# Performance work log

Measured on AMD Instinct MI355X. Metric: run time of the kernel, lower is better.

Reference implementation:

```python
import jax, jax.numpy as jnp
import numpy as np

V, B, C, NS, H, W = 3, 2, 64, 32, 128, 128


def setup_inputs() -> dict:
    key = jax.random.key(0)
    k1, k2 = jax.random.split(key, 2)
    features = jax.random.normal(k1, (V, B, C, H, W), dtype=jnp.float32)
    f = 1.1 * W
    K = np.array([[f, 0.0, (W - 1) / 2.0],
                  [0.0, f, (H - 1) / 2.0],
                  [0.0, 0.0, 1.0]], dtype=np.float32)
    intrinsics = jnp.asarray(np.broadcast_to(K, (V, B, 3, 3)).copy())
    c2w = np.tile(np.eye(4, dtype=np.float32), (V, B, 1, 1))
    rng = np.random.default_rng(0)
    for v in range(1, V):
        for b in range(B):
            th = rng.uniform(-0.03, 0.03)
            Ry = np.array([[np.cos(th), 0.0, np.sin(th)],
                           [0.0, 1.0, 0.0],
                           [-np.sin(th), 0.0, np.cos(th)]], dtype=np.float32)
            c2w[v, b, :3, :3] = Ry
            c2w[v, b, :3, 3] = rng.uniform(-0.1, 0.1, size=3).astype(np.float32)
    cam_to_world = jnp.asarray(c2w)
    scale_hypo = jnp.broadcast_to(jnp.linspace(0.5, 1.5, NS, dtype=jnp.float32), (B, NS)) + jnp.zeros((B, NS), jnp.float32)
    depth_init = 2.0 + 4.0 * jax.random.uniform(k2, (B, H, W), dtype=jnp.float32)
    return {"features": features, "intrinsics": intrinsics, "cam_to_world": cam_to_world,
            "scale_hypo": scale_hypo, "depth_init": depth_init}


def _grid_sample_zeros(feat, grid):
    """torch F.grid_sample(mode='bilinear', padding_mode='zeros', align_corners=False)."""
    Bn, Cn, Hn, Wn = feat.shape
    ix = ((grid[..., 0] + 1.0) * Wn - 1.0) * 0.5
    iy = ((grid[..., 1] + 1.0) * Hn - 1.0) * 0.5
    x0 = jnp.floor(ix); y0 = jnp.floor(iy)
    x1 = x0 + 1.0; y1 = y0 + 1.0
    wx1 = ix - x0; wx0 = 1.0 - wx1
    wy1 = iy - y0; wy0 = 1.0 - wy1
    featf = feat.reshape(Bn, Cn, Hn * Wn)

    def corner(xc, yc, w):
        valid = (xc >= 0) & (xc <= Wn - 1) & (yc >= 0) & (yc <= Hn - 1)
        xi = jnp.clip(xc, 0, Wn - 1).astype(jnp.int32)
        yi = jnp.clip(yc, 0, Hn - 1).astype(jnp.int32)
        idx = (yi * Wn + xi).reshape(Bn, 1, -1)
        v = jnp.take_along_axis(featf, idx, axis=2)  # (B,C,Npts)
        return v * (w * valid).reshape(Bn, 1, -1)

    out = (corner(x0, y0, wx0 * wy0) + corner(x1, y0, wx1 * wy0)
           + corner(x0, y1, wx0 * wy1) + corner(x1, y1, wx1 * wy1))
    return out.reshape(Bn, Cn, grid.shape[1], grid.shape[2])


def _homo_warp(src_feat, scale_hypo, depth_init, src_K, src_c2w, ref_K, ref_c2w):
    # src_feat (B,C,H,W); depth_init (B,1,H,W); returns (B,C,Ns,H,W)
    Bn, Cn, Hn, Wn = src_feat.shape
    Ns = scale_hypo.shape[1]

    def build_grid():
        src_w2c = jnp.linalg.inv(src_c2w)
        ref_w2c = jnp.linalg.inv(ref_c2w)
        # original clones world_to_cam and only replaces the top-left 3x3 with K,
        # so the w2c translation column is kept inside the 'intrinsics' matrix
        src_P = src_w2c.at[:, :3, :3].set(src_K)
        ref_P = ref_w2c.at[:, :3, :3].set(ref_K)
        proj = (src_P @ src_w2c) @ jnp.linalg.inv(ref_P @ ref_w2c)
        rot = proj[:, :3, :3]
        trans = proj[:, :3, 3]
        depth = depth_init.reshape(Bn, 1, 1, Hn * Wn) * scale_hypo[:, None, :, None]  # (B,1,Ns,HW)
        # NOTE: original builds both grid axes from arange(height); valid since H==W
        y, x = jnp.meshgrid(jnp.arange(Hn, dtype=jnp.float32),
                            jnp.arange(Wn, dtype=jnp.float32), indexing='ij')
        xyz = jnp.stack([x.ravel(), y.ravel(), jnp.ones(Hn * Wn, dtype=jnp.float32)])  # (3,HW)
        rot_xyz = jnp.einsum('bij,jn->bin', rot, xyz)                         # (B,3,HW)
        proj_xyz = rot_xyz[:, :, None, :] * depth + trans[:, :, None, None]   # (B,3,Ns,HW)
        proj_xy = proj_xyz[:, :2] / proj_xyz[:, 2:3]
        gx = proj_xy[:, 0] / ((Wn - 1) / 2.0) - 1.0
        gy = proj_xy[:, 1] / ((Hn - 1) / 2.0) - 1.0
        return jnp.stack([gx, gy], axis=-1).reshape(Bn, Ns * Hn, Wn, 2)

    grid = jax.lax.stop_gradient(build_grid())  # torch computes the grid under no_grad
    warped = _grid_sample_zeros(src_feat, grid)
    return warped.reshape(Bn, Cn, Ns, Hn, Wn)


def reference(features, intrinsics, cam_to_world, scale_hypo, depth_init):
    num_views = features.shape[0]
    Bn, Cn, Hn, Wn = features.shape[1:]
    Ns = scale_hypo.shape[1]
    ref_K, ref_c2w = intrinsics[0], cam_to_world[0]
    # faithfully replicate torch's in-place ref_volume.sub_() bug:
    # ref accumulates the subtraction of every previously-warped volume
    ref_running = jnp.broadcast_to(features[0][:, :, None], (Bn, Cn, Ns, Hn, Wn))
    cost = jnp.zeros((Bn, Ns, Hn, Wn), dtype=features.dtype)
    for v in range(1, num_views):
        warped = _homo_warp(features[v], scale_hypo, depth_init[:, None],
                            intrinsics[v], cam_to_world[v], ref_K, ref_c2w)
        ref_running = ref_running - warped
        cost = cost + jnp.sqrt(jnp.sum(ref_running * ref_running, axis=1))  # L2 over C
    cost = cost / (num_views - 1)
    cost = jnp.mean(cost, axis=(2, 3))          # (B, Nscale)
    prob = jax.nn.softmax(cost, axis=1)
    return jnp.sum(prob * scale_hypo, axis=1)   # (B,)
```

## Files before the change

### kernel.cpp

```cpp
#include <hip/hip_runtime.h>
#include <math.h>

constexpr int NV = 3;
constexpr int NB = 2;
constexpr int NC = 64;
constexpr int NSC = 32;
constexpr int NH = 128;
constexpr int NW = 128;
constexpr int NSB = 4;

template <int CTRL>
__device__ __forceinline__ float dpp_add(float x) {
    int s = __builtin_amdgcn_update_dpp(0, __float_as_int(x), CTRL, 0xf, 0xf, true);
    return x + __int_as_float(s);
}

__device__ __forceinline__ void conv8(const uint4& q, float* o) {
    o[0] = __uint_as_float(q.x << 16);
    o[1] = __uint_as_float(q.x & 0xFFFF0000u);
    o[2] = __uint_as_float(q.y << 16);
    o[3] = __uint_as_float(q.y & 0xFFFF0000u);
    o[4] = __uint_as_float(q.z << 16);
    o[5] = __uint_as_float(q.z & 0xFFFF0000u);
    o[6] = __uint_as_float(q.w << 16);
    o[7] = __uint_as_float(q.w & 0xFFFF0000u);
}

__device__ __forceinline__ unsigned int f32_to_bf16_rne(float f) {
    unsigned int u = __float_as_uint(f);
    u += 0x7fffu + ((u >> 16) & 1u);
    return u >> 16;
}

__device__ void inv4x4(const double* m, double* out) {
    double inv[16];
    inv[0]  =  m[5]*m[10]*m[15] - m[5]*m[11]*m[14] - m[9]*m[6]*m[15] + m[9]*m[7]*m[14] + m[13]*m[6]*m[11] - m[13]*m[7]*m[10];
    inv[4]  = -m[4]*m[10]*m[15] + m[4]*m[11]*m[14] + m[8]*m[6]*m[15] - m[8]*m[7]*m[14] - m[12]*m[6]*m[11] + m[12]*m[7]*m[10];
    inv[8]  =  m[4]*m[9]*m[15]  - m[4]*m[11]*m[13] - m[8]*m[5]*m[15] + m[8]*m[7]*m[13] + m[12]*m[5]*m[11] - m[12]*m[7]*m[9];
    inv[12] = -m[4]*m[9]*m[14]  + m[4]*m[10]*m[13] + m[8]*m[5]*m[14] - m[8]*m[6]*m[13] - m[12]*m[5]*m[10] + m[12]*m[6]*m[9];
    inv[1]  = -m[1]*m[10]*m[15] + m[1]*m[11]*m[14] + m[9]*m[2]*m[15] - m[9]*m[3]*m[14] - m[13]*m[2]*m[11] + m[13]*m[3]*m[10];
    inv[5]  =  m[0]*m[10]*m[15] - m[0]*m[11]*m[14] - m[8]*m[2]*m[15] + m[8]*m[3]*m[14] + m[12]*m[2]*m[11] - m[12]*m[3]*m[10];
    inv[9]  = -m[0]*m[9]*m[15]  + m[0]*m[11]*m[13] + m[8]*m[1]*m[15] - m[8]*m[3]*m[13] - m[12]*m[1]*m[11] + m[12]*m[3]*m[9];
    inv[13] =  m[0]*m[9]*m[14]  - m[0]*m[10]*m[13] - m[8]*m[1]*m[14] + m[8]*m[2]*m[13] + m[12]*m[1]*m[10] - m[12]*m[2]*m[9];
    inv[2]  =  m[1]*m[6]*m[15]  - m[1]*m[7]*m[14]  - m[5]*m[2]*m[15] + m[5]*m[3]*m[14] + m[13]*m[2]*m[7]  - m[13]*m[3]*m[6];
    inv[6]  = -m[0]*m[6]*m[15]  + m[0]*m[7]*m[14]  + m[4]*m[2]*m[15] - m[4]*m[3]*m[14] - m[12]*m[2]*m[7]  + m[12]*m[3]*m[6];
    inv[10] =  m[0]*m[5]*m[15]  - m[0]*m[7]*m[13]  - m[4]*m[1]*m[15] + m[4]*m[3]*m[13] + m[12]*m[1]*m[7]  - m[12]*m[3]*m[5];
    inv[14] = -m[0]*m[5]*m[14]  + m[0]*m[6]*m[13]  + m[4]*m[1]*m[14] - m[4]*m[2]*m[13] - m[12]*m[1]*m[6]  + m[12]*m[2]*m[5];
    inv[3]  = -m[1]*m[6]*m[11]  + m[1]*m[7]*m[10]  + m[5]*m[2]*m[11] - m[5]*m[3]*m[10] - m[9]*m[2]*m[7]   + m[9]*m[3]*m[6];
    inv[7]  =  m[0]*m[6]*m[11]  - m[0]*m[7]*m[10]  - m[4]*m[2]*m[11] + m[4]*m[3]*m[10] + m[8]*m[2]*m[7]   - m[8]*m[3]*m[6];
    inv[11] = -m[0]*m[5]*m[11]  + m[0]*m[7]*m[9]   + m[4]*m[1]*m[11] - m[4]*m[3]*m[9]  - m[8]*m[1]*m[7]   + m[8]*m[3]*m[5];
    inv[15] =  m[0]*m[5]*m[10]  - m[0]*m[6]*m[9]   - m[4]*m[1]*m[10] + m[4]*m[2]*m[9]  + m[8]*m[1]*m[6]   - m[8]*m[2]*m[5];
    double det = m[0]*inv[0] + m[1]*inv[4] + m[2]*inv[8] + m[3]*inv[12];
    det = 1.0 / det;
    for (int i = 0; i < 16; ++i) out[i] = inv[i] * det;
}

__device__ void mat4mul(const double* a, const double* b, double* o) {
    for (int i = 0; i < 4; ++i)
        for (int j = 0; j < 4; ++j) {
            double s = 0.0;
            for (int k = 0; k < 4; ++k) s += a[i*4+k] * b[k*4+j];
            o[i*4+j] = s;
        }
}

__global__ void setup_kernel(const float* __restrict__ intr,
                             const float* __restrict__ c2w,
                             float* __restrict__ rt,
                             float* __restrict__ cost) {
    int t = threadIdx.x;
    if (t >= 4 && t < 4 + NB * NSC) cost[t - 4] = 0.f;
    if (t >= 2 * NB) return;
    int vi = t >> 1;
    int b  = t & 1;
    int v  = vi + 1;

    double src_c2w[16], ref_c2w[16];
    for (int i = 0; i < 16; ++i) {
        src_c2w[i] = (double)c2w[(v * NB + b) * 16 + i];
        ref_c2w[i] = (double)c2w[(0 * NB + b) * 16 + i];
    }
    double src_w2c[16], ref_w2c[16];
    inv4x4(src_c2w, src_w2c);
    inv4x4(ref_c2w, ref_w2c);

    double srcP[16], refP[16];
    for (int i = 0; i < 16; ++i) { srcP[i] = src_w2c[i]; refP[i] = ref_w2c[i]; }
    for (int r = 0; r < 3; ++r)
        for (int c = 0; c < 3; ++c) {
            srcP[r*4+c] = (double)intr[(v * NB + b) * 9 + r*3 + c];
            refP[r*4+c] = (double)intr[(0 * NB + b) * 9 + r*3 + c];
        }

    double M1[16], M2[16], M2inv[16];
    mat4mul(srcP, src_w2c, M1);
    mat4mul(refP, ref_w2c, M2);
    inv4x4(M2, M2inv);
    double proj[16];
    mat4mul(M1, M2inv, proj);

    float* o = rt + (vi * NB + b) * 12;
    o[0] = (float)proj[0];  o[1] = (float)proj[1];  o[2]  = (float)proj[2];
    o[3] = (float)proj[4];  o[4] = (float)proj[5];  o[5]  = (float)proj[6];
    o[6] = (float)proj[8];  o[7] = (float)proj[9];  o[8]  = (float)proj[10];
    o[9] = (float)proj[3];  o[10] = (float)proj[7]; o[11] = (float)proj[11];
}

__global__ __launch_bounds__(256) void transpose_kernel(const float* __restrict__ in,
                                                        unsigned int* __restrict__ out) {
    __shared__ float tile[NC][NW + 1];
    const int y  = blockIdx.x;
    const int vb = blockIdx.y;

    for (int i = threadIdx.x; i < NC * NW; i += 256) {
        int c = i >> 7;
        int x = i & (NW - 1);
        tile[c][x] = in[((size_t)(vb * NC + c) * NH + y) * NW + x];
    }
    __syncthreads();
    unsigned int* dst = out + ((size_t)vb * NH + y) * NW * (NC / 2);
    for (int i = threadIdx.x; i < NW * (NC / 2); i += 256) {
        int x  = i >> 5;
        int cp = i & 31;
        unsigned int lo = f32_to_bf16_rne(tile[2 * cp][x]);
        unsigned int hi = f32_to_bf16_rne(tile[2 * cp + 1][x]);
        dst[x * (NC / 2) + cp] = lo | (hi << 16);
    }
}

__global__ __launch_bounds__(256) void cost_kernel(
    const unsigned int* __restrict__ ftb,
    const float* __restrict__ depth,
    const float* __restrict__ scale,
    const float* __restrict__ rt,
    float* __restrict__ cost)
{
    const int tid  = threadIdx.x;
    const int lane = tid & 63;
    const int wv   = tid >> 6;
    const int grp  = lane >> 3;
    const int gl   = lane & 7;
    const int nsg  = blockIdx.y;
    const int b    = blockIdx.z;

    const int p = blockIdx.x * 32 + wv * 8 + grp;
    const int x = p & (NW - 1);
    const int y = p >> 7;
    const float fx = (float)x;
    const float fy = (float)y;

    const float d0 = depth[(b * NH + y) * NW + x];

    const uint4* f0q = (const uint4*)(ftb) + ((size_t)(0 * NB + b) * NH * NW + p) * 8 + gl;
    const uint4* v1q = (const uint4*)(ftb) + ((size_t)(1 * NB + b) * NH * NW) * 8 + gl;
    const uint4* v2q = (const uint4*)(ftb) + ((size_t)(2 * NB + b) * NH * NW) * 8 + gl;

    float f0c[8];
    conv8(*f0q, f0c);

    float R0[12], R1[12];
#pragma unroll
    for (int k = 0; k < 12; ++k) {
        R0[k] = rt[(0 * NB + b) * 12 + k];
        R1[k] = rt[(1 * NB + b) * 12 + k];
    }
    const float ax0 = R0[0] * fx + R0[1] * fy + R0[2];
    const float ay0 = R0[3] * fx + R0[4] * fy + R0[5];
    const float az0 = R0[6] * fx + R0[7] * fy + R0[8];
    const float ax1 = R1[0] * fx + R1[1] * fy + R1[2];
    const float ay1 = R1[3] * fx + R1[4] * fy + R1[5];
    const float az1 = R1[6] * fx + R1[7] * fy + R1[8];

    const float CXY = 64.0f / 63.5f;

    __shared__ float red[4][NSB];
    float outv[NSB];

#pragma unroll
    for (int nsub = 0; nsub < NSB; ++nsub) {
        const float s = scale[b * NSC + nsg * NSB + nsub];
        const float d = d0 * s;

        int   ti[2][4];
        float tw[2][4];
#pragma unroll
        for (int vi = 0; vi < 2; ++vi) {
            float px = (vi ? ax1 : ax0) * d + (vi ? R1[9]  : R0[9]);
            float py = (vi ? ay1 : ay0) * d + (vi ? R1[10] : R0[10]);
            float pz = (vi ? az1 : az0) * d + (vi ? R1[11] : R0[11]);
            float invz = __builtin_amdgcn_rcpf(pz);
            float ix = (px * invz) * CXY - 0.5f;
            float iy = (py * invz) * CXY - 0.5f;

            float x0f = floorf(ix), y0f = floorf(iy);
            float wx1 = ix - x0f, wx0 = 1.f - wx1;
            float wy1 = iy - y0f, wy0 = 1.f - wy1;

            float mx0 = (x0f >= 0.f  && x0f <= 127.f) ? wx0 : 0.f;
            float mx1 = (x0f >= -1.f && x0f <= 126.f) ? wx1 : 0.f;
            float my0 = (y0f >= 0.f  && y0f <= 127.f) ? wy0 : 0.f;
            float my1 = (y0f >= -1.f && y0f <= 126.f) ? wy1 : 0.f;

            int xi0 = (int)fminf(fmaxf(x0f, 0.f), 127.f);
            int yi0 = (int)fminf(fmaxf(y0f, 0.f), 127.f);
            int xo = (x0f >= 0.f && x0f <= 126.f) ? 8 : 0;
            int yo = (y0f >= 0.f && y0f <= 126.f) ? NW * 8 : 0;

            int base = (yi0 * NW + xi0) * 8;
            ti[vi][0] = base;
            ti[vi][1] = base + xo;
            ti[vi][2] = base + yo;
            ti[vi][3] = base + yo + xo;
            tw[vi][0] = mx0 * my0;
            tw[vi][1] = mx1 * my0;
            tw[vi][2] = mx0 * my1;
            tw[vi][3] = mx1 * my1;
        }

        uint4 t0 = v1q[ti[0][0]];
        uint4 t1 = v1q[ti[0][1]];
        uint4 t2 = v1q[ti[0][2]];
        uint4 t3 = v1q[ti[0][3]];
        uint4 u0 = v2q[ti[1][0]];
        uint4 u1 = v2q[ti[1][1]];
        uint4 u2 = v2q[ti[1][2]];
        uint4 u3 = v2q[ti[1][3]];

        float c8[8], acc[8], r[8];

        conv8(t0, acc);
#pragma unroll
        for (int k = 0; k < 8; ++k) acc[k] *= tw[0][0];
        conv8(t1, c8);
#pragma unroll
        for (int k = 0; k < 8; ++k) acc[k] += c8[k] * tw[0][1];
        conv8(t2, c8);
#pragma unroll
        for (int k = 0; k < 8; ++k) acc[k] += c8[k] * tw[0][2];
        conv8(t3, c8);
#pragma unroll
        for (int k = 0; k < 8; ++k) acc[k] += c8[k] * tw[0][3];

        float sq1 = 0.f;
#pragma unroll
        for (int k = 0; k < 8; ++k) {
            r[k] = f0c[k] - acc[k];
            sq1 += r[k] * r[k];
        }

        conv8(u0, acc);
#pragma unroll
        for (int k = 0; k < 8; ++k) acc[k] *= tw[1][0];
        conv8(u1, c8);
#pragma unroll
        for (int k = 0; k < 8; ++k) acc[k] += c8[k] * tw[1][1];
        conv8(u2, c8);
#pragma unroll
        for (int k = 0; k < 8; ++k) acc[k] += c8[k] * tw[1][2];
        conv8(u3, c8);
#pragma unroll
        for (int k = 0; k < 8; ++k) acc[k] += c8[k] * tw[1][3];

        float sq2 = 0.f;
#pragma unroll
        for (int k = 0; k < 8; ++k) {
            r[k] -= acc[k];
            sq2 += r[k] * r[k];
        }

        sq1 = dpp_add<0x111>(sq1);
        sq1 = dpp_add<0x112>(sq1);
        sq1 = dpp_add<0x114>(sq1);
        sq2 = dpp_add<0x111>(sq2);
        sq2 = dpp_add<0x112>(sq2);
        sq2 = dpp_add<0x114>(sq2);
        float sv = sqrtf(sq1) + sqrtf(sq2);
        sv = dpp_add<0x118>(sv);
        sv = dpp_add<0x142>(sv);
        sv = dpp_add<0x143>(sv);
        outv[nsub] = sv;
    }

    if (lane == 63) {
#pragma unroll
        for (int nsub = 0; nsub < NSB; ++nsub) red[wv][nsub] = outv[nsub];
    }
    __syncthreads();
    if (tid < NSB) {
        float t = red[0][tid] + red[1][tid] + red[2][tid] + red[3][tid];
        atomicAdd(&cost[b * NSC + nsg * NSB + tid], t * (0.5f / (float)(NH * NW)));
    }
}

__global__ void finalize_kernel(const float* __restrict__ cost,
                                const float* __restrict__ scale,
                                float* __restrict__ out) {
    int tid = threadIdx.x;
    if (tid >= NB * NSC) return;
    int b = tid >> 5;
    int ns = tid & 31;
    float c = cost[b * NSC + ns];
    float sv = scale[b * NSC + ns];

    float m = c;
#pragma unroll
    for (int mk = 1; mk < 32; mk <<= 1) m = fmaxf(m, __shfl_xor(m, mk, 64));
    float e = __expf(c - m);
    float sum = e;
#pragma unroll
    for (int mk = 1; mk < 32; mk <<= 1) sum += __shfl_xor(sum, mk, 64);
    float val = (e / sum) * sv;
#pragma unroll
    for (int mk = 1; mk < 32; mk <<= 1) val += __shfl_xor(val, mk, 64);
    if (ns == 0) out[b] = val;
}

extern "C" void kernel_launch(void* const* d_in, const int* in_sizes, int n_in,
                              void* d_out, int out_size, void* d_ws, size_t ws_size,
                              hipStream_t stream) {
    const float* features   = (const float*)d_in[0];
    const float* intrinsics = (const float*)d_in[1];
    const float* cam2world  = (const float*)d_in[2];
    const float* scale_hypo = (const float*)d_in[3];
    const float* depth_init = (const float*)d_in[4];
    float* out = (float*)d_out;

    unsigned int* ftb = (unsigned int*)d_ws;
    float* rt   = (float*)(ftb + (size_t)NV * NB * NH * NW * (NC / 2));
    float* cost = rt + 2 * NB * 12;

    setup_kernel<<<1, 128, 0, stream>>>(intrinsics, cam2world, rt, cost);

    dim3 tgrid(NH, NV * NB);
    transpose_kernel<<<tgrid, 256, 0, stream>>>(features, ftb);

    dim3 cgrid(NH * NW / 32, NSC / NSB, NB);
    cost_kernel<<<cgrid, 256, 0, stream>>>(ftb, depth_init, scale_hypo, rt, cost);

    finalize_kernel<<<1, 64, 0, stream>>>(cost, scale_hypo, out);
}
```

Measured before the change: 187.8 us.

## Switch feature staging to fp16 with packed math and fold setup into transpose

Features are now stored as packed fp16 instead of bf16, and the bilinear interpolation and residual run in packed half2 arithmetic. Squared norms use the fdot2 instruction, which removes the per-element unpack to fp32. The separate setup kernel that computes the projection matrices and zeroes the cost buffer is merged into one block of the transpose kernel, saving a launch. The cost is lower precision: interpolation now accumulates in fp16 and the weights are rounded to fp16.

Result: faster. 166.0 us (-11.6%).

```diff
diff --git a/kernel.cpp b/kernel.cpp
--- a/kernel.cpp
+++ b/kernel.cpp
@@ -9,27 +9,21 @@
 constexpr int NW = 128;
 constexpr int NSB = 4;
 
+typedef _Float16 h2_t __attribute__((ext_vector_type(2)));
+
 template <int CTRL>
 __device__ __forceinline__ float dpp_add(float x) {
     int s = __builtin_amdgcn_update_dpp(0, __float_as_int(x), CTRL, 0xf, 0xf, true);
     return x + __int_as_float(s);
 }
 
-__device__ __forceinline__ void conv8(const uint4& q, float* o) {
-    o[0] = __uint_as_float(q.x << 16);
-    o[1] = __uint_as_float(q.x & 0xFFFF0000u);
-    o[2] = __uint_as_float(q.y << 16);
-    o[3] = __uint_as_float(q.y & 0xFFFF0000u);
-    o[4] = __uint_as_float(q.z << 16);
-    o[5] = __uint_as_float(q.z & 0xFFFF0000u);
-    o[6] = __uint_as_float(q.w << 16);
-    o[7] = __uint_as_float(q.w & 0xFFFF0000u);
-}
-
-__device__ __forceinline__ unsigned int f32_to_bf16_rne(float f) {
-    unsigned int u = __float_as_uint(f);
-    u += 0x7fffu + ((u >> 16) & 1u);
-    return u >> 16;
+__device__ __forceinline__ float dot2acc(h2_t a, float acc) {
+#if __has_builtin(__builtin_amdgcn_fdot2)
+    return __builtin_amdgcn_fdot2(a, a, acc, false);
+#else
+    float x = (float)a.x, y = (float)a.y;
+    return acc + x * x + y * y;
+#endif
 }
 
 __device__ void inv4x4(const double* m, double* out) {
@@ -64,50 +58,12 @@
         }
 }
 
-__global__ void setup_kernel(const float* __restrict__ intr,
-                             const float* __restrict__ c2w,
-                             float* __restrict__ rt,
-                             float* __restrict__ cost) {
-    int t = threadIdx.x;
-    if (t >= 4 && t < 4 + NB * NSC) cost[t - 4] = 0.f;
-    if (t >= 2 * NB) return;
-    int vi = t >> 1;
-    int b  = t & 1;
-    int v  = vi + 1;
-
-    double src_c2w[16], ref_c2w[16];
-    for (int i = 0; i < 16; ++i) {
-        src_c2w[i] = (double)c2w[(v * NB + b) * 16 + i];
-        ref_c2w[i] = (double)c2w[(0 * NB + b) * 16 + i];
-    }
-    double src_w2c[16], ref_w2c[16];
-    inv4x4(src_c2w, src_w2c);
-    inv4x4(ref_c2w, ref_w2c);
-
-    double srcP[16], refP[16];
-    for (int i = 0; i < 16; ++i) { srcP[i] = src_w2c[i]; refP[i] = ref_w2c[i]; }
-    for (int r = 0; r < 3; ++r)
-        for (int c = 0; c < 3; ++c) {
-            srcP[r*4+c] = (double)intr[(v * NB + b) * 9 + r*3 + c];
-            refP[r*4+c] = (double)intr[(0 * NB + b) * 9 + r*3 + c];
-        }
-
-    double M1[16], M2[16], M2inv[16];
-    mat4mul(srcP, src_w2c, M1);
-    mat4mul(refP, ref_w2c, M2);
-    inv4x4(M2, M2inv);
-    double proj[16];
-    mat4mul(M1, M2inv, proj);
-
-    float* o = rt + (vi * NB + b) * 12;
-    o[0] = (float)proj[0];  o[1] = (float)proj[1];  o[2]  = (float)proj[2];
-    o[3] = (float)proj[4];  o[4] = (float)proj[5];  o[5]  = (float)proj[6];
-    o[6] = (float)proj[8];  o[7] = (float)proj[9];  o[8]  = (float)proj[10];
-    o[9] = (float)proj[3];  o[10] = (float)proj[7]; o[11] = (float)proj[11];
-}
-
 __global__ __launch_bounds__(256) void transpose_kernel(const float* __restrict__ in,
-                                                        unsigned int* __restrict__ out) {
+                                                        unsigned int* __restrict__ out,
+                                                        const float* __restrict__ intr,
+                                                        const float* __restrict__ c2w,
+                                                        float* __restrict__ rt,
+                                                        float* __restrict__ cost) {
     __shared__ float tile[NC][NW + 1];
     const int y  = blockIdx.x;
     const int vb = blockIdx.y;
@@ -122,9 +78,48 @@
     for (int i = threadIdx.x; i < NW * (NC / 2); i += 256) {
         int x  = i >> 5;
         int cp = i & 31;
-        unsigned int lo = f32_to_bf16_rne(tile[2 * cp][x]);
-        unsigned int hi = f32_to_bf16_rne(tile[2 * cp + 1][x]);
-        dst[x * (NC / 2) + cp] = lo | (hi << 16);
+        h2_t h = { (_Float16)tile[2 * cp][x], (_Float16)tile[2 * cp + 1][x] };
+        dst[x * (NC / 2) + cp] = __builtin_bit_cast(unsigned int, h);
+    }
+
+    if (blockIdx.x == 0 && blockIdx.y == 0) {
+        int t = threadIdx.x;
+        if (t >= 4 && t < 4 + NB * NSC) cost[t - 4] = 0.f;
+        if (t < 2 * NB) {
+            int vi = t >> 1;
+            int b  = t & 1;
+            int v  = vi + 1;
+
+            double src_c2w[16], ref_c2w[16];
+            for (int i = 0; i < 16; ++i) {
+                src_c2w[i] = (double)c2w[(v * NB + b) * 16 + i];
+                ref_c2w[i] = (double)c2w[(0 * NB + b) * 16 + i];
+            }
+            double src_w2c[16], ref_w2c[16];
+            inv4x4(src_c2w, src_w2c);
+            inv4x4(ref_c2w, ref_w2c);
+
+            double srcP[16], refP[16];
+            for (int i = 0; i < 16; ++i) { srcP[i] = src_w2c[i]; refP[i] = ref_w2c[i]; }
+            for (int r = 0; r < 3; ++r)
+                for (int c = 0; c < 3; ++c) {
+                    srcP[r*4+c] = (double)intr[(v * NB + b) * 9 + r*3 + c];
+                    refP[r*4+c] = (double)intr[(0 * NB + b) * 9 + r*3 + c];
+                }
+
+            double M1[16], M2[16], M2inv[16];
+            mat4mul(srcP, src_w2c, M1);
+            mat4mul(refP, ref_w2c, M2);
+            inv4x4(M2, M2inv);
+            double proj[16];
+            mat4mul(M1, M2inv, proj);
+
+            float* o = rt + (vi * NB + b) * 12;
+            o[0] = (float)proj[0];  o[1] = (float)proj[1];  o[2]  = (float)proj[2];
+            o[3] = (float)proj[4];  o[4] = (float)proj[5];  o[5]  = (float)proj[6];
+            o[6] = (float)proj[8];  o[7] = (float)proj[9];  o[8]  = (float)proj[10];
+            o[9] = (float)proj[3];  o[10] = (float)proj[7]; o[11] = (float)proj[11];
+        }
     }
 }
 
@@ -155,8 +150,8 @@
     const uint4* v1q = (const uint4*)(ftb) + ((size_t)(1 * NB + b) * NH * NW) * 8 + gl;
     const uint4* v2q = (const uint4*)(ftb) + ((size_t)(2 * NB + b) * NH * NW) * 8 + gl;
 
-    float f0c[8];
-    conv8(*f0q, f0c);
+    const uint4 f0u = *f0q;
+    const h2_t* f0h = (const h2_t*)&f0u;
 
     float R0[12], R1[12];
 #pragma unroll
@@ -226,46 +221,42 @@
         uint4 u2 = v2q[ti[1][2]];
         uint4 u3 = v2q[ti[1][3]];
 
-        float c8[8], acc[8], r[8];
-
-        conv8(t0, acc);
-#pragma unroll
-        for (int k = 0; k < 8; ++k) acc[k] *= tw[0][0];
-        conv8(t1, c8);
-#pragma unroll
-        for (int k = 0; k < 8; ++k) acc[k] += c8[k] * tw[0][1];
-        conv8(t2, c8);
-#pragma unroll
-        for (int k = 0; k < 8; ++k) acc[k] += c8[k] * tw[0][2];
-        conv8(t3, c8);
-#pragma unroll
-        for (int k = 0; k < 8; ++k) acc[k] += c8[k] * tw[0][3];
-
-        float sq1 = 0.f;
-#pragma unroll
-        for (int k = 0; k < 8; ++k) {
-            r[k] = f0c[k] - acc[k];
-            sq1 += r[k] * r[k];
-        }
-
-        conv8(u0, acc);
-#pragma unroll
-        for (int k = 0; k < 8; ++k) acc[k] *= tw[1][0];
-        conv8(u1, c8);
-#pragma unroll
-        for (int k = 0; k < 8; ++k) acc[k] += c8[k] * tw[1][1];
-        conv8(u2, c8);
-#pragma unroll
-        for (int k = 0; k < 8; ++k) acc[k] += c8[k] * tw[1][2];
-        conv8(u3, c8);
-#pragma unroll
-        for (int k = 0; k < 8; ++k) acc[k] += c8[k] * tw[1][3];
-
-        float sq2 = 0.f;
-#pragma unroll
-        for (int k = 0; k < 8; ++k) {
-            r[k] -= acc[k];
-            sq2 += r[k] * r[k];
+        _Float16 w00 = (_Float16)(-tw[0][0]), w01 = (_Float16)(-tw[0][1]);
+        _Float16 w02 = (_Float16)(-tw[0][2]), w03 = (_Float16)(-tw[0][3]);
+        _Float16 w10 = (_Float16)(-tw[1][0]), w11 = (_Float16)(-tw[1][1]);
+        _Float16 w12 = (_Float16)(-tw[1][2]), w13 = (_Float16)(-tw[1][3]);
+        h2_t h00 = {w00, w00}, h01 = {w01, w01}, h02 = {w02, w02}, h03 = {w03, w03};
+        h2_t h10 = {w10, w10}, h11 = {w11, w11}, h12 = {w12, w12}, h13 = {w13, w13};
+
+        const h2_t* p0 = (const h2_t*)&t0;
+        const h2_t* p1 = (const h2_t*)&t1;
+        const h2_t* p2 = (const h2_t*)&t2;
+        const h2_t* p3 = (const h2_t*)&t3;
+        const h2_t* q0 = (const h2_t*)&u0;
+        const h2_t* q1 = (const h2_t*)&u1;
+        const h2_t* q2 = (const h2_t*)&u2;
+        const h2_t* q3 = (const h2_t*)&u3;
+
+        h2_t r[4];
+        float sq1 = 0.f, sq2 = 0.f;
+#pragma unroll
+        for (int j = 0; j < 4; ++j) {
+            h2_t rr = f0h[j];
+            rr += p0[j] * h00;
+            rr += p1[j] * h01;
+            rr += p2[j] * h02;
+            rr += p3[j] * h03;
+            r[j] = rr;
+            sq1 = dot2acc(rr, sq1);
+        }
+#pragma unroll
+        for (int j = 0; j < 4; ++j) {
+            h2_t rr = r[j];
+            rr += q0[j] * h10;
+            rr += q1[j] * h11;
+            rr += q2[j] * h12;
+            rr += q3[j] * h13;
+            sq2 = dot2acc(rr, sq2);
         }
 
         sq1 = dpp_add<0x111>(sq1);
@@ -329,10 +320,8 @@
     float* rt   = (float*)(ftb + (size_t)NV * NB * NH * NW * (NC / 2));
     float* cost = rt + 2 * NB * 12;
 
-    setup_kernel<<<1, 128, 0, stream>>>(intrinsics, cam2world, rt, cost);
-
     dim3 tgrid(NH, NV * NB);
-    transpose_kernel<<<tgrid, 256, 0, stream>>>(features, ftb);
+    transpose_kernel<<<tgrid, 256, 0, stream>>>(features, ftb, intrinsics, cam2world, rt, cost);
 
     dim3 cgrid(NH * NW / 32, NSC / NSB, NB);
     cost_kernel<<<cgrid, 256, 0, stream>>>(ftb, depth_init, scale_hypo, rt, cost);
```
